# Optimization experiments

Measured on AMD Instinct MI355X. Metric: run time of the kernel, lower is better.

## Reference

```python
import jax, jax.numpy as jnp
import numpy as np
import math

B, LAT, HID, T, NCLS = 128, 128, 256, 1920, 3
EPS = 1e-5


def _ln(x, g, b):
    m = jnp.mean(x, axis=-1, keepdims=True)
    v = jnp.var(x, axis=-1, keepdims=True)
    return (x - m) * jax.lax.rsqrt(v + EPS) * g + b


def _leaky(x):
    return jax.nn.leaky_relu(x, 0.2)


def _lstm_layer(x, Wih, Whh, bih, bhh):
    # x: [T, B, D] time-major; gate order i,f,g,o (PyTorch convention)
    xw = jnp.einsum('tbd,gd->tbg', x, Wih) + bih + bhh  # precompute input projection
    Hd = Whh.shape[1]
    bsz = x.shape[1]

    def step(carry, xg):
        h, c = carry
        gates = xg + h @ Whh.T
        i, f, g, o = jnp.split(gates, 4, axis=-1)
        c = jax.nn.sigmoid(f) * c + jax.nn.sigmoid(i) * jnp.tanh(g)
        h = jax.nn.sigmoid(o) * jnp.tanh(c)
        return (h, c), h

    init = (jnp.zeros((bsz, Hd), x.dtype), jnp.zeros((bsz, Hd), x.dtype))
    _, hs = jax.lax.scan(step, init, xw)
    return hs  # [T, B, H]


def setup_inputs() -> dict:
    key = jax.random.key(0)
    ks = jax.random.split(key, 16)
    s = 0.05
    H2 = HID // 2
    d = {
        'z': jax.random.normal(ks[0], (B, LAT), jnp.float32),
        'labels': jax.random.randint(ks[1], (B,), 0, 4, jnp.int64),
        'emb_W': jax.random.normal(ks[2], (NCLS + 1, HID), jnp.float32) * s,
        'np_W': jax.random.normal(ks[3], (HID, LAT + HID), jnp.float32) * s,
        'np_b': jnp.zeros((HID,), jnp.float32),
        'np_g': jnp.ones((HID,), jnp.float32),
        'np_be': jnp.zeros((HID,), jnp.float32),
        'Wih0': jax.random.normal(ks[4], (4 * HID, 2 * HID), jnp.float32) * s,
        'Whh0': jax.random.normal(ks[5], (4 * HID, HID), jnp.float32) * s,
        'bih0': jnp.zeros((4 * HID,), jnp.float32),
        'bhh0': jnp.zeros((4 * HID,), jnp.float32),
        'Wih1': jax.random.normal(ks[6], (4 * HID, HID), jnp.float32) * s,
        'Whh1': jax.random.normal(ks[7], (4 * HID, HID), jnp.float32) * s,
        'bih1': jnp.zeros((4 * HID,), jnp.float32),
        'bhh1': jnp.zeros((4 * HID,), jnp.float32),
        'oW1': jax.random.normal(ks[8], (H2, HID), jnp.float32) * s,
        'ob1': jnp.zeros((H2,), jnp.float32),
        'og': jnp.ones((H2,), jnp.float32),
        'obe': jnp.zeros((H2,), jnp.float32),
        'oW2': jax.random.normal(ks[9], (3, H2), jnp.float32) * s,
        'ob2': jnp.zeros((3,), jnp.float32),
        'sW1': jax.random.normal(ks[10], (H2, HID), jnp.float32) * s,
        'sb1': jnp.zeros((H2,), jnp.float32),
        'sg': jnp.ones((H2,), jnp.float32),
        'sbe': jnp.zeros((H2,), jnp.float32),
        'sW2': jax.random.normal(ks[11], (1, H2), jnp.float32) * s,
        'sb2': jnp.zeros((1,), jnp.float32),
        'stress_w': jnp.array(1.8, jnp.float32),
        'amu_w': jnp.array([0.15, 0.7, 0.15], jnp.float32),
        'amu_b': jnp.array(-0.3, jnp.float32),
    }
    return d


def reference(z, labels, emb_W, np_W, np_b, np_g, np_be, Wih0, Whh0, bih0, bhh0,
              Wih1, Whh1, bih1, bhh1, oW1, ob1, og, obe, oW2, ob2,
              sW1, sb1, sg, sbe, sW2, sb2, stress_w, amu_w, amu_b):
    bsz = z.shape[0]
    emb = emb_W[labels]                                   # [B, H]
    h = _leaky(_ln(jnp.concatenate([z, emb], axis=1) @ np_W.T + np_b, np_g, np_be))
    # [B, T, 2H]
    sig_in = jnp.concatenate([
        jnp.broadcast_to(h[:, None, :], (bsz, T, HID)),
        jnp.broadcast_to(emb[:, None, :], (bsz, T, HID)),
    ], axis=2)
    x = jnp.transpose(sig_in, (1, 0, 2))                  # time-major [T, B, 2H]
    x = _lstm_layer(x, Wih0, Whh0, bih0, bhh0)
    x = _lstm_layer(x, Wih1, Whh1, bih1, bhh1)
    ch = jnp.transpose(x, (1, 0, 2))                      # [B, T, H]

    # oscillation params per sample (vectorized over batch)
    h_avg = jnp.mean(ch, axis=1)                          # [B, H]
    op = _leaky(_ln(h_avg @ oW1.T + ob1, og, obe)) @ oW2.T + ob2  # [B, 3]
    freq = 0.23 + 0.04 * jnp.tanh(op[:, 0])
    amp = 2.0 + 1.5 * jnp.tanh(op[:, 1])
    phase = math.pi * jax.nn.sigmoid(op[:, 2])
    t = jnp.linspace(0.0, 1.0, T)
    osc = amp[:, None] * jnp.sin(2.0 * math.pi * freq[:, None] * T * t[None, :] + phase[:, None])  # [B, T]

    base = jnp.tanh(_leaky(_ln(ch @ sW1.T + sb1, sg, sbe)) @ sW2.T + sb2)  # [B, T, 1]
    enhanced = 0.6 * base[..., 0] + 0.4 * osc             # [B, T]

    stressed = stress_w * enhanced                        # conv1d k=1, w=1.8
    xp = jnp.pad(enhanced, ((0, 0), (1, 1)))
    smoothed = amu_w[0] * xp[:, :-2] + amu_w[1] * xp[:, 1:-1] + amu_w[2] * xp[:, 2:] + amu_b

    lab = labels[:, None]
    out = jnp.where(lab == 1, enhanced,
          jnp.where(lab == 2, stressed,
          jnp.where(lab == 3, smoothed, jnp.zeros_like(enhanced))))
    return out[..., None]                                  # [B, T, 1]
```

## Files before the change

kernel.cpp:

```cpp
#include <hip/hip_runtime.h>

#define TSTEPS 1920
#define NB 128
#define HIDN 256
#define LATN 128
#define EPSF 1e-5f

typedef __attribute__((ext_vector_type(8))) short bf16x8;
typedef __attribute__((ext_vector_type(4))) float f32x4;

__device__ __forceinline__ unsigned short f2bf(float x) {
    unsigned u = __builtin_bit_cast(unsigned, x);
    unsigned r = (u + 0x7fffu + ((u >> 16) & 1u)) >> 16;
    return (unsigned short)r;
}
__device__ __forceinline__ float bf2f(unsigned short h) {
    unsigned u = ((unsigned)h) << 16;
    return __builtin_bit_cast(float, u);
}
__device__ __forceinline__ float fsig(float x) {
    float e = __expf(-fabsf(x));
    float s = 1.f / (1.f + e);
    return x >= 0.f ? s : 1.f - s;
}
__device__ __forceinline__ float ftanh(float x) {
    float e = __expf(-2.f * fabsf(x));
    float r = (1.f - e) / (1.f + e);
    return x >= 0.f ? r : -r;
}
__device__ __forceinline__ float fleaky(float x) { return x > 0.f ? x : 0.2f * x; }
__device__ __forceinline__ bf16x8 bcast16(uint4 v) { return __builtin_bit_cast(bf16x8, v); }

__device__ __forceinline__ unsigned aload(const unsigned* p) {
    return __hip_atomic_load(p, __ATOMIC_RELAXED, __HIP_MEMORY_SCOPE_AGENT);
}
__device__ __forceinline__ void astore(unsigned* p, unsigned v) {
    __hip_atomic_store(p, v, __ATOMIC_RELAXED, __HIP_MEMORY_SCOPE_AGENT);
}

#define MFMA(a, b, c) __builtin_amdgcn_mfma_f32_16x16x32_bf16((a), (b), (c), 0, 0, 0)

#define FLG(ph, g, s) (((ph) * 8 + (g)) * 8 + (s)) * 32
#define HPLANE(g, layer, buf) (((g) * 2 + (layer)) * 2 + (buf)) * 4096

__global__ void init_sync(unsigned* hbuf, unsigned* flags) {
    int i = blockIdx.x * 256 + threadIdx.x;
    if (i < 131072) hbuf[i] = 0u;
    if (i < 4096) flags[i] = 0u;
}

__global__ void pack_bfrag_sliced(const float* __restrict__ A, const float* __restrict__ Bsrc,
                                  int KA, int KB,
                                  unsigned short* __restrict__ hi, unsigned short* __restrict__ lo) {
    int e = blockIdx.x * 256 + threadIdx.x;
    int K = KA + KB;
    int KT = K >> 5;
    if (e >= 1024 * K) return;
    int j = e & 7;
    int l = (e >> 3) & 63;
    int r = e >> 9;
    int kt = r % KT;
    int r2 = r / KT;
    int v = r2 & 7;
    int w = r2 >> 3;
    int n = (v >> 1) * 256 + 32 * w + 16 * (v & 1) + (l & 15);
    int k = kt * 32 + (l >> 4) * 8 + j;
    float val = (k < KA) ? A[n * KA + k] : Bsrc[n * KB + (k - KA)];
    unsigned short h = f2bf(val);
    hi[e] = h;
    lo[e] = f2bf(val - bf2f(h));
}

__global__ void pack_sw1kj(const float* __restrict__ sW1, unsigned short* __restrict__ out) {
    int e = blockIdx.x * 256 + threadIdx.x;
    if (e >= 256 * 128) return;
    int j = e & 127, k = e >> 7;
    out[e] = f2bf(sW1[j * 256 + k]);
}

__global__ void pack4T(const float* __restrict__ W, int N, int K, float* __restrict__ out) {
    int e = blockIdx.x * 256 + threadIdx.x;
    if (e >= N * K) return;
    int j = e & 3;
    int rest = e >> 2;
    int n = rest % N;
    int k4 = rest / N;
    out[e] = W[n * K + 4 * k4 + j];
}

__global__ void prep_b1(const float* __restrict__ bih1, const float* __restrict__ bhh1,
                        float* __restrict__ b1sum) {
    int i = blockIdx.x * 256 + threadIdx.x;
    if (i < 1024) b1sum[i] = bih1[i] + bhh1[i];
}

__global__ void np_head(const float* __restrict__ z, const int* __restrict__ labels,
                        const float* __restrict__ emb_W, const float* __restrict__ np_W,
                        const float* __restrict__ np_b, const float* __restrict__ np_g,
                        const float* __restrict__ np_be, float* __restrict__ x_const) {
    int b = blockIdx.x;
    int j = threadIdx.x;
    __shared__ float xc[LATN + HIDN];
    __shared__ float red[8];
    int lab = labels[b];
    if (j < LATN) xc[j] = z[b * LATN + j];
    float e = emb_W[lab * HIDN + j];
    xc[LATN + j] = e;
    __syncthreads();
    float d = np_b[j];
    for (int k = 0; k < LATN + HIDN; ++k) d += xc[k] * np_W[j * (LATN + HIDN) + k];
    int lane = j & 63, wv = j >> 6;
    float s = d, s2 = d * d;
    for (int o = 1; o < 64; o <<= 1) { s += __shfl_xor(s, o); s2 += __shfl_xor(s2, o); }
    if (lane == 0) { red[wv] = s; red[4 + wv] = s2; }
    __syncthreads();
    float S = red[0] + red[1] + red[2] + red[3];
    float S2 = red[4] + red[5] + red[6] + red[7];
    float m = S * (1.f / 256.f);
    float var = S2 * (1.f / 256.f) - m * m;
    float h = fleaky((d - m) * rsqrtf(var + EPSF) * np_g[j] + np_be[j]);
    x_const[b * 512 + j] = h;
    x_const[b * 512 + 256 + j] = e;
}

__global__ void __launch_bounds__(1024) xw0_kernel(const float* __restrict__ x_const,
                                                   const float4* __restrict__ Wih0T4,
                                                   const float* __restrict__ bih0,
                                                   const float* __restrict__ bhh0,
                                                   float* __restrict__ xw0) {
    int b = blockIdx.x;
    int g = threadIdx.x;
    __shared__ float xc[512];
    if (g < 512) xc[g] = x_const[b * 512 + g];
    __syncthreads();
    const float4* xc4 = (const float4*)xc;
    float4 acc = {0.f, 0.f, 0.f, 0.f};
#pragma unroll 8
    for (int k4 = 0; k4 < 128; ++k4) {
        float4 w = Wih0T4[k4 * 1024 + g];
        float4 x = xc4[k4];
        acc.x = fmaf(w.x, x.x, acc.x);
        acc.y = fmaf(w.y, x.y, acc.y);
        acc.z = fmaf(w.z, x.z, acc.z);
        acc.w = fmaf(w.w, x.w, acc.w);
    }
    xw0[b * 1024 + g] = bih0[g] + bhh0[g] + ((acc.x + acc.y) + (acc.z + acc.w));
}

__global__ void __launch_bounds__(512, 2) lstm_coop(
    const uint4* __restrict__ whh0h, const uint4* __restrict__ whh0l,
    const uint4* __restrict__ w1h, const uint4* __restrict__ w1l,
    const unsigned short* __restrict__ sw1kj_g, const float* __restrict__ xw0g,
    const float* __restrict__ b1sum, const float* __restrict__ sb1,
    const float* __restrict__ sg, const float* __restrict__ sbe,
    const float* __restrict__ sW2, const float* __restrict__ sb2,
    unsigned* __restrict__ hbuf, unsigned* __restrict__ flags,
    float* __restrict__ base_out, float* __restrict__ hsum_out) {
    extern __shared__ char smem[];
    unsigned short* hhi = (unsigned short*)smem;
    unsigned short* hlo = (unsigned short*)(smem + 16384);
    unsigned short* sw1s = (unsigned short*)(smem + 32768);
    float* gatesL = (float*)(smem + 98304);
    float* ppart = (float*)(smem + 106752);
    char* hhiB = smem;
    char* hloB = smem + 16384;

    const int gidx = blockIdx.x & 7;
    const int W = blockIdx.x >> 3;
    const int g16 = gidx * 16;
    const int tid = threadIdx.x;
    const int l = tid & 63;
    const int v = tid >> 6;
    const int ln16 = l & 15;
    const int kg = l >> 4;

    for (int i = tid; i < 256 * 128; i += 512) sw1s[i] = sw1kj_g[i];
    for (int i = tid; i < 8192; i += 512) { hhi[i] = 0; hlo[i] = 0; }

    uint4 b0h[8], b0l[8];
#pragma unroll
    for (int kt = 0; kt < 8; ++kt) {
        int idx = ((W * 8 + v) * 8 + kt) * 64 + l;
        b0h[kt] = whh0h[idx];
        b0l[kt] = whh0l[idx];
    }
    const uint4* w1hb = w1h + ((W * 8 + v) * 16) * 64 + l;
    const uint4* w1lb = w1l + ((W * 8 + v) * 16) * 64 + l;

    const int row = tid >> 5;
    const int ul = tid & 31;
    const int ug = 32 * W + ul;
    float xwi[4], b1v[4];
#pragma unroll
    for (int gt = 0; gt < 4; ++gt) {
        xwi[gt] = xw0g[(g16 + row) * 1024 + gt * 256 + ug];
        b1v[gt] = b1sum[gt * 256 + ug];
    }
    float c0 = 0.f, c1 = 0.f, hs = 0.f;

    const float sb1a = sb1[l], sb1b = sb1[64 + l];
    const float sga = sg[l], sgb = sg[64 + l];
    const float sbea = sbe[l], sbeb = sbe[64 + l];
    const float sw2a = sW2[l], sw2b = sW2[64 + l];
    const float sb2v = sb2[0];

    unsigned* h0buf[2] = {hbuf + HPLANE(gidx, 0, 0), hbuf + HPLANE(gidx, 0, 1)};
    unsigned* h1buf[2] = {hbuf + HPLANE(gidx, 1, 0), hbuf + HPLANE(gidx, 1, 1)};
    unsigned* fl0 = flags + FLG(0, gidx, W);
    unsigned* fl1 = flags + FLG(1, gidx, W);
    unsigned* fl0base = flags + FLG(0, gidx, 0);
    unsigned* fl1base = flags + FLG(1, gidx, 0);

    const int abase = ln16 * 1024;
    const int aswz = (ln16 & 7) << 4;
    const int kgo = kg * 16;
    const int gcol = (v >> 1) * 32 + (v & 1) * 16 + ln16;
    const int hprow = 2 * W + (v & 1);
    const int hpswz = (hprow & 7) << 4;
    const int kq = v >> 1;

    __syncthreads();

    for (int t = 0; t < TSTEPS; ++t) {
        const int cur = t & 1, prev = cur ^ 1;
        {
            unsigned* src = h1buf[prev];
            for (int i = tid; i < 4096; i += 512) {
                int r_ = i >> 8, u_ = i & 255;
                unsigned val = aload(src + i);
                int off = r_ * 1024 + ((512 + 2 * u_) ^ ((r_ & 7) << 4));
                *(unsigned short*)(hhiB + off) = (unsigned short)(val >> 16);
                *(unsigned short*)(hloB + off) = (unsigned short)(val & 0xffffu);
            }
        }
        __syncthreads();
        {
            f32x4 acc = {0.f, 0.f, 0.f, 0.f};
#pragma unroll
            for (int kt = 0; kt < 8; ++kt) {
                int aoff = abase + ((kt * 64 + kgo) ^ aswz);
                bf16x8 ahi = bcast16(*(const uint4*)(hhiB + aoff));
                bf16x8 alo = bcast16(*(const uint4*)(hloB + aoff));
                bf16x8 bh = bcast16(b0h[kt]);
                bf16x8 bl = bcast16(b0l[kt]);
                acc = MFMA(ahi, bh, acc);
                acc = MFMA(alo, bh, acc);
                acc = MFMA(ahi, bl, acc);
            }
#pragma unroll
            for (int r = 0; r < 4; ++r) gatesL[(kg * 4 + r) * 132 + gcol] = acc[r];
        }
        if (t > 0) {
            float accA = 0.f, accB = 0.f;
            int hb = hprow * 1024;
#pragma unroll 4
            for (int k = kq * 64; k < kq * 64 + 64; ++k) {
                int off = hb + ((512 + 2 * k) ^ hpswz);
                float h = bf2f(*(const unsigned short*)(hhiB + off)) +
                          bf2f(*(const unsigned short*)(hloB + off));
                float wA = bf2f(sw1s[k * 128 + l]);
                float wB = bf2f(sw1s[k * 128 + 64 + l]);
                accA = fmaf(wA, h, accA);
                accB = fmaf(wB, h, accB);
            }
            ppart[(v & 1) * 512 + kq * 128 + l] = accA;
            ppart[(v & 1) * 512 + kq * 128 + 64 + l] = accB;
        }
        __syncthreads();
        {
            float i_ = gatesL[row * 132 + ul] + xwi[0];
            float f_ = gatesL[row * 132 + 32 + ul] + xwi[1];
            float g_ = gatesL[row * 132 + 64 + ul] + xwi[2];
            float o_ = gatesL[row * 132 + 96 + ul] + xwi[3];
            c0 = fsig(f_) * c0 + fsig(i_) * ftanh(g_);
            float h = fsig(o_) * ftanh(c0);
            unsigned short hh = f2bf(h);
            unsigned short ll = f2bf(h - bf2f(hh));
            astore(h0buf[cur] + row * 256 + ug, ((unsigned)hh << 16) | (unsigned)ll);
        }
        asm volatile("s_waitcnt vmcnt(0)" ::: "memory");
        __syncthreads();
        if (tid == 0) astore(fl0, (unsigned)(t + 1));
        {
            unsigned tgt = (unsigned)(t + 1);
            while (true) {
                unsigned val = (l < 8) ? aload(fl0base + l * 32) : tgt;
                if (__all((int)(val >= tgt))) break;
                __builtin_amdgcn_s_sleep(1);
            }
        }
        asm volatile("" ::: "memory");
        {
            unsigned* src = h0buf[cur];
            for (int i = tid; i < 4096; i += 512) {
                int r_ = i >> 8, u_ = i & 255;
                unsigned val = aload(src + i);
                int off = r_ * 1024 + ((2 * u_) ^ ((r_ & 7) << 4));
                *(unsigned short*)(hhiB + off) = (unsigned short)(val >> 16);
                *(unsigned short*)(hloB + off) = (unsigned short)(val & 0xffffu);
            }
        }
        __syncthreads();
        {
            f32x4 acc = {0.f, 0.f, 0.f, 0.f};
#pragma unroll 4
            for (int kt = 0; kt < 16; ++kt) {
                int aoff = abase + ((kt * 64 + kgo) ^ aswz);
                bf16x8 ahi = bcast16(*(const uint4*)(hhiB + aoff));
                bf16x8 alo = bcast16(*(const uint4*)(hloB + aoff));
                bf16x8 bh = bcast16(w1hb[kt * 64]);
                bf16x8 bl = bcast16(w1lb[kt * 64]);
                acc = MFMA(ahi, bh, acc);
                acc = MFMA(alo, bh, acc);
                acc = MFMA(ahi, bl, acc);
            }
#pragma unroll
            for (int r = 0; r < 4; ++r) gatesL[(kg * 4 + r) * 132 + gcol] = acc[r];
        }
        __syncthreads();
        {
            float i_ = gatesL[row * 132 + ul] + b1v[0];
            float f_ = gatesL[row * 132 + 32 + ul] + b1v[1];
            float g_ = gatesL[row * 132 + 64 + ul] + b1v[2];
            float o_ = gatesL[row * 132 + 96 + ul] + b1v[3];
            c1 = fsig(f_) * c1 + fsig(i_) * ftanh(g_);
            float h = fsig(o_) * ftanh(c1);
            hs += h;
            unsigned short hh = f2bf(h);
            unsigned short ll = f2bf(h - bf2f(hh));
            astore(h1buf[cur] + row * 256 + ug, ((unsigned)hh << 16) | (unsigned)ll);
        }
        if (t > 0 && v < 2) {
            float sA = sb1a, sB = sb1b;
#pragma unroll
            for (int q = 0; q < 4; ++q) {
                sA += ppart[v * 512 + q * 128 + l];
                sB += ppart[v * 512 + q * 128 + 64 + l];
            }
            float ssum = sA + sB, ssq = sA * sA + sB * sB;
#pragma unroll
            for (int o = 1; o < 64; o <<= 1) { ssum += __shfl_xor(ssum, o); ssq += __shfl_xor(ssq, o); }
            float m = ssum * (1.f / 128.f);
            float var = ssq * (1.f / 128.f) - m * m;
            float rstd = rsqrtf(var + EPSF);
            float p0 = fleaky((sA - m) * rstd * sga + sbea);
            float p1 = fleaky((sB - m) * rstd * sgb + sbeb);
            float q = p0 * sw2a + p1 * sw2b;
#pragma unroll
            for (int o = 1; o < 64; o <<= 1) q += __shfl_xor(q, o);
            if (l == 0) base_out[(g16 + 2 * W + v) * TSTEPS + (t - 1)] = ftanh(q + sb2v);
        }
        asm volatile("s_waitcnt vmcnt(0)" ::: "memory");
        __syncthreads();
        if (tid == 0) astore(fl1, (unsigned)(t + 1));
        {
            unsigned tgt = (unsigned)(t + 1);
            while (true) {
                unsigned val = (l < 8) ? aload(fl1base + l * 32) : tgt;
                if (__all((int)(val >= tgt))) break;
                __builtin_amdgcn_s_sleep(1);
            }
        }
        asm volatile("" ::: "memory");
    }
    {
        unsigned* src = h1buf[(TSTEPS - 1) & 1];
        for (int i = tid; i < 4096; i += 512) {
            int r_ = i >> 8, u_ = i & 255;
            unsigned val = aload(src + i);
            int off = r_ * 1024 + ((512 + 2 * u_) ^ ((r_ & 7) << 4));
            *(unsigned short*)(hhiB + off) = (unsigned short)(val >> 16);
            *(unsigned short*)(hloB + off) = (unsigned short)(val & 0xffffu);
        }
    }
    __syncthreads();
    {
        float accA = 0.f, accB = 0.f;
        int hb = hprow * 1024;
#pragma unroll 4
        for (int k = kq * 64; k < kq * 64 + 64; ++k) {
            int off = hb + ((512 + 2 * k) ^ hpswz);
            float h = bf2f(*(const unsigned short*)(hhiB + off)) +
                      bf2f(*(const unsigned short*)(hloB + off));
            accA = fmaf(bf2f(sw1s[k * 128 + l]), h, accA);
            accB = fmaf(bf2f(sw1s[k * 128 + 64 + l]), h, accB);
        }
        ppart[(v & 1) * 512 + kq * 128 + l] = accA;
        ppart[(v & 1) * 512 + kq * 128 + 64 + l] = accB;
    }
    __syncthreads();
    if (v < 2) {
        float sA = sb1a, sB = sb1b;
#pragma unroll
        for (int q = 0; q < 4; ++q) {
            sA += ppart[v * 512 + q * 128 + l];
            sB += ppart[v * 512 + q * 128 + 64 + l];
        }
        float ssum = sA + sB, ssq = sA * sA + sB * sB;
#pragma unroll
        for (int o = 1; o < 64; o <<= 1) { ssum += __shfl_xor(ssum, o); ssq += __shfl_xor(ssq, o); }
        float m = ssum * (1.f / 128.f);
        float var = ssq * (1.f / 128.f) - m * m;
        float rstd = rsqrtf(var + EPSF);
        float p0 = fleaky((sA - m) * rstd * sga + sbea);
        float p1 = fleaky((sB - m) * rstd * sgb + sbeb);
        float q = p0 * sw2a + p1 * sw2b;
#pragma unroll
        for (int o = 1; o < 64; o <<= 1) q += __shfl_xor(q, o);
        if (l == 0) base_out[(g16 + 2 * W + v) * TSTEPS + (TSTEPS - 1)] = ftanh(q + sb2v);
    }
    hsum_out[(g16 + row) * HIDN + ug] = hs;
}

__global__ void out_kernel(const float* __restrict__ hsum, const float* __restrict__ oW1,
                           const float* __restrict__ ob1, const float* __restrict__ og,
                           const float* __restrict__ obe, const float* __restrict__ oW2,
                           const float* __restrict__ ob2, const float* __restrict__ base,
                           const int* __restrict__ labels, const float* __restrict__ stress_w,
                           const float* __restrict__ amu_w, const float* __restrict__ amu_b,
                           float* __restrict__ out) {
    int b = blockIdx.x;
    int tid = threadIdx.x;
    int lane = tid & 63, wv = tid >> 6;
    __shared__ float havg[256];
    __shared__ float red[8];
    __shared__ float params[3];
    __shared__ float e_row[TSTEPS];
    havg[tid] = hsum[b * 256 + tid] * (1.f / (float)TSTEPS);
    __syncthreads();
    float d1 = 0.f;
    if (tid < 128) {
        d1 = ob1[tid];
        for (int k = 0; k < 256; ++k) d1 += havg[k] * oW1[tid * 256 + k];
    }
    float s = d1, s2 = d1 * d1;
    for (int o = 1; o < 64; o <<= 1) { s += __shfl_xor(s, o); s2 += __shfl_xor(s2, o); }
    if (lane == 0 && wv < 2) { red[wv] = s; red[2 + wv] = s2; }
    __syncthreads();
    float m = (red[0] + red[1]) * (1.f / 128.f);
    float var = (red[2] + red[3]) * (1.f / 128.f) - m * m;
    float rstd = rsqrtf(var + EPSF);
    float p = 0.f;
    if (tid < 128) p = fleaky((d1 - m) * rstd * og[tid] + obe[tid]);
    float q0 = tid < 128 ? p * oW2[0 * 128 + tid] : 0.f;
    float q1 = tid < 128 ? p * oW2[1 * 128 + tid] : 0.f;
    float q2 = tid < 128 ? p * oW2[2 * 128 + tid] : 0.f;
    for (int o = 1; o < 64; o <<= 1) {
        q0 += __shfl_xor(q0, o); q1 += __shfl_xor(q1, o); q2 += __shfl_xor(q2, o);
    }
    __syncthreads();
    if (lane == 0 && wv < 2) { red[wv] = q0; red[2 + wv] = q1; red[4 + wv] = q2; }
    __syncthreads();
    if (tid == 0) {
        float op0 = red[0] + red[1] + ob2[0];
        float op1 = red[2] + red[3] + ob2[1];
        float op2 = red[4] + red[5] + ob2[2];
        params[0] = 0.23f + 0.04f * ftanh(op0);
        params[1] = 2.0f + 1.5f * ftanh(op1);
        params[2] = 3.14159265358979f * fsig(op2);
    }
    __syncthreads();
    float freq = params[0], amp = params[1], ph = params[2];
    for (int t = tid; t < TSTEPS; t += 256) {
        float x = freq * ((float)TSTEPS * (float)t / (float)(TSTEPS - 1));
        x -= floorf(x);
        float osc = amp * __sinf(6.28318530717958647f * x + ph);
        e_row[t] = 0.6f * base[b * TSTEPS + t] + 0.4f * osc;
    }
    __syncthreads();
    int lab = labels[b];
    float sw = stress_w[0];
    float w0 = amu_w[0], w1 = amu_w[1], w2 = amu_w[2], ab = amu_b[0];
    for (int t = tid; t < TSTEPS; t += 256) {
        float e = e_row[t];
        float r;
        if (lab == 1) r = e;
        else if (lab == 2) r = sw * e;
        else if (lab == 3) {
            float em = t > 0 ? e_row[t - 1] : 0.f;
            float ep = t < TSTEPS - 1 ? e_row[t + 1] : 0.f;
            r = w0 * em + w1 * e + w2 * ep + ab;
        } else r = 0.f;
        out[b * TSTEPS + t] = r;
    }
}

extern "C" void kernel_launch(void* const* d_in, const int* in_sizes, int n_in,
                              void* d_out, int out_size, void* d_ws, size_t ws_size,
                              hipStream_t stream) {
    (void)in_sizes; (void)n_in; (void)out_size; (void)ws_size;
    const float* z      = (const float*)d_in[0];
    const int* labels   = (const int*)d_in[1];
    const float* emb_W  = (const float*)d_in[2];
    const float* np_W   = (const float*)d_in[3];
    const float* np_b   = (const float*)d_in[4];
    const float* np_g   = (const float*)d_in[5];
    const float* np_be  = (const float*)d_in[6];
    const float* Wih0   = (const float*)d_in[7];
    const float* Whh0   = (const float*)d_in[8];
    const float* bih0   = (const float*)d_in[9];
    const float* bhh0   = (const float*)d_in[10];
    const float* Wih1   = (const float*)d_in[11];
    const float* Whh1   = (const float*)d_in[12];
    const float* bih1   = (const float*)d_in[13];
    const float* bhh1   = (const float*)d_in[14];
    const float* oW1    = (const float*)d_in[15];
    const float* ob1    = (const float*)d_in[16];
    const float* og     = (const float*)d_in[17];
    const float* obe    = (const float*)d_in[18];
    const float* oW2    = (const float*)d_in[19];
    const float* ob2    = (const float*)d_in[20];
    const float* sW1    = (const float*)d_in[21];
    const float* sb1    = (const float*)d_in[22];
    const float* sg     = (const float*)d_in[23];
    const float* sbe    = (const float*)d_in[24];
    const float* sW2    = (const float*)d_in[25];
    const float* sb2    = (const float*)d_in[26];
    const float* stressw= (const float*)d_in[27];
    const float* amu_w  = (const float*)d_in[28];
    const float* amu_b  = (const float*)d_in[29];
    float* out = (float*)d_out;

    uint8_t* ws = (uint8_t*)d_ws;
    size_t off = 0;
    unsigned short* whh0h = (unsigned short*)(ws + off); off += (size_t)1024 * 256 * 2;
    unsigned short* whh0l = (unsigned short*)(ws + off); off += (size_t)1024 * 256 * 2;
    unsigned short* w1h   = (unsigned short*)(ws + off); off += (size_t)1024 * 512 * 2;
    unsigned short* w1l   = (unsigned short*)(ws + off); off += (size_t)1024 * 512 * 2;
    unsigned short* sw1kj = (unsigned short*)(ws + off); off += (size_t)256 * 128 * 2;
    float* Wih0T4 = (float*)(ws + off); off += (size_t)1024 * 512 * 4;
    float* x_const= (float*)(ws + off); off += (size_t)NB * 512 * 4;
    float* xw0    = (float*)(ws + off); off += (size_t)NB * 1024 * 4;
    float* b1sum  = (float*)(ws + off); off += (size_t)1024 * 4;
    float* hsum   = (float*)(ws + off); off += (size_t)NB * 256 * 4;
    float* basef  = (float*)(ws + off); off += (size_t)NB * TSTEPS * 4;
    off = (off + 255) & ~(size_t)255;
    unsigned* hbuf = (unsigned*)(ws + off); off += (size_t)131072 * 4;
    unsigned* flags= (unsigned*)(ws + off); off += (size_t)4096 * 4;

    init_sync<<<512, 256, 0, stream>>>(hbuf, flags);
    pack_bfrag_sliced<<<1024, 256, 0, stream>>>(Whh0, nullptr, 256, 0, whh0h, whh0l);
    pack_bfrag_sliced<<<2048, 256, 0, stream>>>(Wih1, Whh1, 256, 256, w1h, w1l);
    pack_sw1kj<<<128, 256, 0, stream>>>(sW1, sw1kj);
    pack4T<<<2048, 256, 0, stream>>>(Wih0, 1024, 512, Wih0T4);
    prep_b1<<<4, 256, 0, stream>>>(bih1, bhh1, b1sum);

    np_head<<<NB, 256, 0, stream>>>(z, labels, emb_W, np_W, np_b, np_g, np_be, x_const);
    xw0_kernel<<<NB, 1024, 0, stream>>>(x_const, (const float4*)Wih0T4, bih0, bhh0, xw0);
    lstm_coop<<<64, 512, 110848, stream>>>((const uint4*)whh0h, (const uint4*)whh0l,
                                           (const uint4*)w1h, (const uint4*)w1l,
                                           sw1kj, xw0, b1sum, sb1, sg, sbe, sW2, sb2,
                                           hbuf, flags, basef, hsum);
    out_kernel<<<NB, 256, 0, stream>>>(hsum, oW1, ob1, og, obe, oW2, ob2, basef, labels,
                                       stressw, amu_w, amu_b, out);
}
```

Measured before the change: 23.98 ms.

## Wavefront-pipeline LSTM layers with one grid barrier per step

Layer 1's step t-1 now runs in the same phase as layer 0's step t. Both read one staged buffer holding h0 and h1, which cuts the cross-block flag barriers from two per timestep to one. Layer-1 weights are kept in registers instead of being reloaded from global memory each step. The sW1 head projection now runs on MFMA over a repacked fragment layout instead of scalar FMA. The changes add register pressure and more LDS, and shift the head computation by one phase.

```diff
diff --git a/kernel.cpp b/kernel.cpp
--- a/kernel.cpp
+++ b/kernel.cpp
@@ -34,13 +34,16 @@
 __device__ __forceinline__ unsigned aload(const unsigned* p) {
     return __hip_atomic_load(p, __ATOMIC_RELAXED, __HIP_MEMORY_SCOPE_AGENT);
 }
+__device__ __forceinline__ unsigned long long aload64(const unsigned long long* p) {
+    return __hip_atomic_load(p, __ATOMIC_RELAXED, __HIP_MEMORY_SCOPE_AGENT);
+}
 __device__ __forceinline__ void astore(unsigned* p, unsigned v) {
     __hip_atomic_store(p, v, __ATOMIC_RELAXED, __HIP_MEMORY_SCOPE_AGENT);
 }
 
 #define MFMA(a, b, c) __builtin_amdgcn_mfma_f32_16x16x32_bf16((a), (b), (c), 0, 0, 0)
 
-#define FLG(ph, g, s) (((ph) * 8 + (g)) * 8 + (s)) * 32
+#define FLG(g, s) ((g) * 8 + (s)) * 32
 #define HPLANE(g, layer, buf) (((g) * 2 + (layer)) * 2 + (buf)) * 4096
 
 __global__ void init_sync(unsigned* hbuf, unsigned* flags) {
@@ -71,11 +74,16 @@
     lo[e] = f2bf(val - bf2f(h));
 }
 
-__global__ void pack_sw1kj(const float* __restrict__ sW1, unsigned short* __restrict__ out) {
+__global__ void pack_sw1frag(const float* __restrict__ sW1, unsigned short* __restrict__ out) {
     int e = blockIdx.x * 256 + threadIdx.x;
-    if (e >= 256 * 128) return;
-    int j = e & 127, k = e >> 7;
-    out[e] = f2bf(sW1[j * 256 + k]);
+    if (e >= 32768) return;
+    int j3 = e & 7;
+    int l = (e >> 3) & 63;
+    int r = e >> 9;
+    int kt = r & 7, w = r >> 3;
+    int n = w * 16 + (l & 15);
+    int k = kt * 32 + (l >> 4) * 8 + j3;
+    out[e] = f2bf(sW1[n * 256 + k]);
 }
 
 __global__ void pack4T(const float* __restrict__ W, int N, int K, float* __restrict__ out) {
@@ -150,20 +158,19 @@
 __global__ void __launch_bounds__(512, 2) lstm_coop(
     const uint4* __restrict__ whh0h, const uint4* __restrict__ whh0l,
     const uint4* __restrict__ w1h, const uint4* __restrict__ w1l,
-    const unsigned short* __restrict__ sw1kj_g, const float* __restrict__ xw0g,
+    const unsigned short* __restrict__ sw1f_g, const float* __restrict__ xw0g,
     const float* __restrict__ b1sum, const float* __restrict__ sb1,
     const float* __restrict__ sg, const float* __restrict__ sbe,
     const float* __restrict__ sW2, const float* __restrict__ sb2,
     unsigned* __restrict__ hbuf, unsigned* __restrict__ flags,
     float* __restrict__ base_out, float* __restrict__ hsum_out) {
     extern __shared__ char smem[];
-    unsigned short* hhi = (unsigned short*)smem;
-    unsigned short* hlo = (unsigned short*)(smem + 16384);
-    unsigned short* sw1s = (unsigned short*)(smem + 32768);
-    float* gatesL = (float*)(smem + 98304);
-    float* ppart = (float*)(smem + 106752);
-    char* hhiB = smem;
-    char* hloB = smem + 16384;
+    char* pHhi = smem;
+    char* pHlo = smem + 16384;
+    unsigned short* sw1f = (unsigned short*)(smem + 32768);
+    float* gates0 = (float*)(smem + 98304);
+    float* gates1 = (float*)(smem + 106752);
+    float* s1b = (float*)(smem + 115200);
 
     const int gidx = blockIdx.x & 7;
     const int W = blockIdx.x >> 3;
@@ -174,8 +181,8 @@
     const int ln16 = l & 15;
     const int kg = l >> 4;
 
-    for (int i = tid; i < 256 * 128; i += 512) sw1s[i] = sw1kj_g[i];
-    for (int i = tid; i < 8192; i += 512) { hhi[i] = 0; hlo[i] = 0; }
+    for (int i = tid; i < 16384; i += 512)
+        ((unsigned*)sw1f)[i] = ((const unsigned*)sw1f_g)[i];
 
     uint4 b0h[8], b0l[8];
 #pragma unroll
@@ -184,8 +191,13 @@
         b0h[kt] = whh0h[idx];
         b0l[kt] = whh0l[idx];
     }
-    const uint4* w1hb = w1h + ((W * 8 + v) * 16) * 64 + l;
-    const uint4* w1lb = w1l + ((W * 8 + v) * 16) * 64 + l;
+    uint4 w1hR[16], w1lR[16];
+#pragma unroll
+    for (int kt = 0; kt < 16; ++kt) {
+        int idx = ((W * 8 + v) * 16 + kt) * 64 + l;
+        w1hR[kt] = w1h[idx];
+        w1lR[kt] = w1l[idx];
+    }
 
     const int row = tid >> 5;
     const int ul = tid & 31;
@@ -198,218 +210,170 @@
     }
     float c0 = 0.f, c1 = 0.f, hs = 0.f;
 
-    const float sb1a = sb1[l], sb1b = sb1[64 + l];
-    const float sga = sg[l], sgb = sg[64 + l];
-    const float sbea = sbe[l], sbeb = sbe[64 + l];
-    const float sw2a = sW2[l], sw2b = sW2[64 + l];
+    const float sb1a = sb1[2 * l], sb1b = sb1[2 * l + 1];
+    const float sga = sg[2 * l], sgb = sg[2 * l + 1];
+    const float sbea = sbe[2 * l], sbeb = sbe[2 * l + 1];
+    const float sw2a = sW2[2 * l], sw2b = sW2[2 * l + 1];
     const float sb2v = sb2[0];
 
     unsigned* h0buf[2] = {hbuf + HPLANE(gidx, 0, 0), hbuf + HPLANE(gidx, 0, 1)};
     unsigned* h1buf[2] = {hbuf + HPLANE(gidx, 1, 0), hbuf + HPLANE(gidx, 1, 1)};
-    unsigned* fl0 = flags + FLG(0, gidx, W);
-    unsigned* fl1 = flags + FLG(1, gidx, W);
-    unsigned* fl0base = flags + FLG(0, gidx, 0);
-    unsigned* fl1base = flags + FLG(1, gidx, 0);
+    unsigned* fl = flags + FLG(gidx, W);
+    unsigned* flbase = flags + FLG(gidx, 0);
 
     const int abase = ln16 * 1024;
     const int aswz = (ln16 & 7) << 4;
     const int kgo = kg * 16;
     const int gcol = (v >> 1) * 32 + (v & 1) * 16 + ln16;
-    const int hprow = 2 * W + (v & 1);
-    const int hpswz = (hprow & 7) << 4;
-    const int kq = v >> 1;
-
-    __syncthreads();
-
-    for (int t = 0; t < TSTEPS; ++t) {
-        const int cur = t & 1, prev = cur ^ 1;
+
+#define WAITF(tgtv)                                                              \
+    {                                                                            \
+        unsigned tgt = (unsigned)(tgtv);                                         \
+        while (true) {                                                           \
+            unsigned val = (l < 8) ? aload(flbase + l * 32) : tgt;               \
+            if (__all((int)(val >= tgt))) break;                                 \
+            __builtin_amdgcn_s_sleep(1);                                         \
+        }                                                                        \
+    }                                                                            \
+    asm volatile("" ::: "memory");
+
+#define STAGE2(src0, src1)                                                       \
+    {                                                                            \
+        const unsigned long long* sA = (const unsigned long long*)(src0);        \
+        const unsigned long long* sB = (const unsigned long long*)(src1);        \
+        _Pragma("unroll")                                                        \
+        for (int it = 0; it < 4; ++it) {                                         \
+            int i2 = tid + 512 * it;                                             \
+            int r_ = i2 >> 7, u2 = i2 & 127;                                     \
+            int swz = (r_ & 7) << 4;                                             \
+            int off0 = r_ * 1024 + ((4 * u2) ^ swz);                             \
+            unsigned long long vA = aload64(sA + r_ * 128 + u2);                 \
+            unsigned a0 = (unsigned)vA, a1 = (unsigned)(vA >> 32);               \
+            *(unsigned*)(pHhi + off0) = (a0 >> 16) | (a1 & 0xffff0000u);         \
+            *(unsigned*)(pHlo + off0) = (a0 & 0xffffu) | (a1 << 16);             \
+            int off1 = r_ * 1024 + ((512 + 4 * u2) ^ swz);                       \
+            unsigned long long vB = aload64(sB + r_ * 128 + u2);                 \
+            unsigned e0 = (unsigned)vB, e1 = (unsigned)(vB >> 32);               \
+            *(unsigned*)(pHhi + off1) = (e0 >> 16) | (e1 & 0xffff0000u);         \
+            *(unsigned*)(pHlo + off1) = (e0 & 0xffffu) | (e1 << 16);             \
+        }                                                                        \
+    }
+
+#define HEADFIN(tout)                                                            \
+    if (v < 4) {                                                                 \
+        _Pragma("unroll")                                                        \
+        for (int r4 = 0; r4 < 4; ++r4) {                                         \
+            int hrw = v * 4 + r4;                                                \
+            float2 sv = *(const float2*)&s1b[hrw * 132 + 2 * l];                 \
+            float sA = sv.x + sb1a, sB = sv.y + sb1b;                            \
+            float ssum = sA + sB, ssq = sA * sA + sB * sB;                       \
+            _Pragma("unroll")                                                    \
+            for (int o = 1; o < 64; o <<= 1) {                                   \
+                ssum += __shfl_xor(ssum, o); ssq += __shfl_xor(ssq, o);          \
+            }                                                                    \
+            float m = ssum * (1.f / 128.f);                                      \
+            float var = ssq * (1.f / 128.f) - m * m;                             \
+            float rstd = rsqrtf(var + EPSF);                                     \
+            float p0 = fleaky((sA - m) * rstd * sga + sbea);                     \
+            float p1 = fleaky((sB - m) * rstd * sgb + sbeb);                     \
+            float qd = p0 * sw2a + p1 * sw2b;                                    \
+            _Pragma("unroll")                                                    \
+            for (int o = 1; o < 64; o <<= 1) qd += __shfl_xor(qd, o);            \
+            if (l == 0) base_out[(g16 + hrw) * TSTEPS + (tout)] = ftanh(qd + sb2v); \
+        }                                                                        \
+    }
+
+    __syncthreads();
+
+    for (int p = 0; p <= TSTEPS; ++p) {
+        WAITF(p);
+        STAGE2(h0buf[(p - 1) & 1], h1buf[p & 1]);
+        __syncthreads();
         {
-            unsigned* src = h1buf[prev];
-            for (int i = tid; i < 4096; i += 512) {
-                int r_ = i >> 8, u_ = i & 255;
-                unsigned val = aload(src + i);
-                int off = r_ * 1024 + ((512 + 2 * u_) ^ ((r_ & 7) << 4));
-                *(unsigned short*)(hhiB + off) = (unsigned short)(val >> 16);
-                *(unsigned short*)(hloB + off) = (unsigned short)(val & 0xffffu);
+            f32x4 a0 = {0.f, 0.f, 0.f, 0.f};
+            f32x4 a1 = {0.f, 0.f, 0.f, 0.f};
+            f32x4 ah = {0.f, 0.f, 0.f, 0.f};
+#pragma unroll
+            for (int kt = 0; kt < 8; ++kt) {
+                int aoff = abase + ((kt * 64 + kgo) ^ aswz);
+                bf16x8 ahi = bcast16(*(const uint4*)(pHhi + aoff));
+                bf16x8 alo = bcast16(*(const uint4*)(pHlo + aoff));
+                bf16x8 bh = bcast16(b0h[kt]);
+                bf16x8 bl = bcast16(b0l[kt]);
+                a0 = MFMA(ahi, bh, a0); a0 = MFMA(alo, bh, a0); a0 = MFMA(ahi, bl, a0);
+                bf16x8 ch = bcast16(w1hR[kt]);
+                bf16x8 cl = bcast16(w1lR[kt]);
+                a1 = MFMA(ahi, ch, a1); a1 = MFMA(alo, ch, a1); a1 = MFMA(ahi, cl, a1);
+            }
+#pragma unroll
+            for (int kt = 8; kt < 16; ++kt) {
+                int aoff = abase + ((kt * 64 + kgo) ^ aswz);
+                bf16x8 ahi = bcast16(*(const uint4*)(pHhi + aoff));
+                bf16x8 alo = bcast16(*(const uint4*)(pHlo + aoff));
+                bf16x8 ch = bcast16(w1hR[kt]);
+                bf16x8 cl = bcast16(w1lR[kt]);
+                a1 = MFMA(ahi, ch, a1); a1 = MFMA(alo, ch, a1); a1 = MFMA(ahi, cl, a1);
+                bf16x8 bsw = bcast16(*(const uint4*)&sw1f[((v * 8 + (kt - 8)) * 64 + l) * 8]);
+                ah = MFMA(ahi, bsw, ah); ah = MFMA(alo, bsw, ah);
+            }
+#pragma unroll
+            for (int r = 0; r < 4; ++r) {
+                gates0[(kg * 4 + r) * 132 + gcol] = a0[r];
+                gates1[(kg * 4 + r) * 132 + gcol] = a1[r];
+                s1b[(kg * 4 + r) * 132 + v * 16 + ln16] = ah[r];
             }
         }
         __syncthreads();
         {
-            f32x4 acc = {0.f, 0.f, 0.f, 0.f};
-#pragma unroll
-            for (int kt = 0; kt < 8; ++kt) {
-                int aoff = abase + ((kt * 64 + kgo) ^ aswz);
-                bf16x8 ahi = bcast16(*(const uint4*)(hhiB + aoff));
-                bf16x8 alo = bcast16(*(const uint4*)(hloB + aoff));
-                bf16x8 bh = bcast16(b0h[kt]);
-                bf16x8 bl = bcast16(b0l[kt]);
-                acc = MFMA(ahi, bh, acc);
-                acc = MFMA(alo, bh, acc);
-                acc = MFMA(ahi, bl, acc);
-            }
-#pragma unroll
-            for (int r = 0; r < 4; ++r) gatesL[(kg * 4 + r) * 132 + gcol] = acc[r];
-        }
-        if (t > 0) {
-            float accA = 0.f, accB = 0.f;
-            int hb = hprow * 1024;
-#pragma unroll 4
-            for (int k = kq * 64; k < kq * 64 + 64; ++k) {
-                int off = hb + ((512 + 2 * k) ^ hpswz);
-                float h = bf2f(*(const unsigned short*)(hhiB + off)) +
-                          bf2f(*(const unsigned short*)(hloB + off));
-                float wA = bf2f(sw1s[k * 128 + l]);
-                float wB = bf2f(sw1s[k * 128 + 64 + l]);
-                accA = fmaf(wA, h, accA);
-                accB = fmaf(wB, h, accB);
-            }
-            ppart[(v & 1) * 512 + kq * 128 + l] = accA;
-            ppart[(v & 1) * 512 + kq * 128 + 64 + l] = accB;
-        }
-        __syncthreads();
-        {
-            float i_ = gatesL[row * 132 + ul] + xwi[0];
-            float f_ = gatesL[row * 132 + 32 + ul] + xwi[1];
-            float g_ = gatesL[row * 132 + 64 + ul] + xwi[2];
-            float o_ = gatesL[row * 132 + 96 + ul] + xwi[3];
+            float i_ = gates0[row * 132 + ul] + xwi[0];
+            float f_ = gates0[row * 132 + 32 + ul] + xwi[1];
+            float g_ = gates0[row * 132 + 64 + ul] + xwi[2];
+            float o_ = gates0[row * 132 + 96 + ul] + xwi[3];
             c0 = fsig(f_) * c0 + fsig(i_) * ftanh(g_);
             float h = fsig(o_) * ftanh(c0);
             unsigned short hh = f2bf(h);
             unsigned short ll = f2bf(h - bf2f(hh));
-            astore(h0buf[cur] + row * 256 + ug, ((unsigned)hh << 16) | (unsigned)ll);
+            astore(h0buf[p & 1] + row * 256 + ug, ((unsigned)hh << 16) | (unsigned)ll);
         }
-        asm volatile("s_waitcnt vmcnt(0)" ::: "memory");
-        __syncthreads();
-        if (tid == 0) astore(fl0, (unsigned)(t + 1));
-        {
-            unsigned tgt = (unsigned)(t + 1);
-            while (true) {
-                unsigned val = (l < 8) ? aload(fl0base + l * 32) : tgt;
-                if (__all((int)(val >= tgt))) break;
-                __builtin_amdgcn_s_sleep(1);
-            }
-        }
-        asm volatile("" ::: "memory");
-        {
-            unsigned* src = h0buf[cur];
-            for (int i = tid; i < 4096; i += 512) {
-                int r_ = i >> 8, u_ = i & 255;
-                unsigned val = aload(src + i);
-                int off = r_ * 1024 + ((2 * u_) ^ ((r_ & 7) << 4));
-                *(unsigned short*)(hhiB + off) = (unsigned short)(val >> 16);
-                *(unsigned short*)(hloB + off) = (unsigned short)(val & 0xffffu);
-            }
-        }
-        __syncthreads();
-        {
-            f32x4 acc = {0.f, 0.f, 0.f, 0.f};
-#pragma unroll 4
-            for (int kt = 0; kt < 16; ++kt) {
-                int aoff = abase + ((kt * 64 + kgo) ^ aswz);
-                bf16x8 ahi = bcast16(*(const uint4*)(hhiB + aoff));
-                bf16x8 alo = bcast16(*(const uint4*)(hloB + aoff));
-                bf16x8 bh = bcast16(w1hb[kt * 64]);
-                bf16x8 bl = bcast16(w1lb[kt * 64]);
-                acc = MFMA(ahi, bh, acc);
-                acc = MFMA(alo, bh, acc);
-                acc = MFMA(ahi, bl, acc);
-            }
-#pragma unroll
-            for (int r = 0; r < 4; ++r) gatesL[(kg * 4 + r) * 132 + gcol] = acc[r];
-        }
-        __syncthreads();
-        {
-            float i_ = gatesL[row * 132 + ul] + b1v[0];
-            float f_ = gatesL[row * 132 + 32 + ul] + b1v[1];
-            float g_ = gatesL[row * 132 + 64 + ul] + b1v[2];
-            float o_ = gatesL[row * 132 + 96 + ul] + b1v[3];
+        if (p > 0) {
+            float i_ = gates1[row * 132 + ul] + b1v[0];
+            float f_ = gates1[row * 132 + 32 + ul] + b1v[1];
+            float g_ = gates1[row * 132 + 64 + ul] + b1v[2];
+            float o_ = gates1[row * 132 + 96 + ul] + b1v[3];
             c1 = fsig(f_) * c1 + fsig(i_) * ftanh(g_);
             float h = fsig(o_) * ftanh(c1);
             hs += h;
             unsigned short hh = f2bf(h);
             unsigned short ll = f2bf(h - bf2f(hh));
-            astore(h1buf[cur] + row * 256 + ug, ((unsigned)hh << 16) | (unsigned)ll);
-        }
-        if (t > 0 && v < 2) {
-            float sA = sb1a, sB = sb1b;
-#pragma unroll
-            for (int q = 0; q < 4; ++q) {
-                sA += ppart[v * 512 + q * 128 + l];
-                sB += ppart[v * 512 + q * 128 + 64 + l];
-            }
-            float ssum = sA + sB, ssq = sA * sA + sB * sB;
-#pragma unroll
-            for (int o = 1; o < 64; o <<= 1) { ssum += __shfl_xor(ssum, o); ssq += __shfl_xor(ssq, o); }
-            float m = ssum * (1.f / 128.f);
-            float var = ssq * (1.f / 128.f) - m * m;
-            float rstd = rsqrtf(var + EPSF);
-            float p0 = fleaky((sA - m) * rstd * sga + sbea);
-            float p1 = fleaky((sB - m) * rstd * sgb + sbeb);
-            float q = p0 * sw2a + p1 * sw2b;
-#pragma unroll
-            for (int o = 1; o < 64; o <<= 1) q += __shfl_xor(q, o);
-            if (l == 0) base_out[(g16 + 2 * W + v) * TSTEPS + (t - 1)] = ftanh(q + sb2v);
+            astore(h1buf[(p - 1) & 1] + row * 256 + ug, ((unsigned)hh << 16) | (unsigned)ll);
         }
         asm volatile("s_waitcnt vmcnt(0)" ::: "memory");
         __syncthreads();
-        if (tid == 0) astore(fl1, (unsigned)(t + 1));
-        {
-            unsigned tgt = (unsigned)(t + 1);
-            while (true) {
-                unsigned val = (l < 8) ? aload(fl1base + l * 32) : tgt;
-                if (__all((int)(val >= tgt))) break;
-                __builtin_amdgcn_s_sleep(1);
-            }
+        if (tid == 0) astore(fl, (unsigned)(p + 1));
+        if (p >= 2) HEADFIN(p - 2);
+    }
+    WAITF(TSTEPS + 1);
+    STAGE2(h0buf[(TSTEPS + 1 - 1) & 1], h1buf[(TSTEPS + 1) & 1]);
+    __syncthreads();
+    {
+        f32x4 ah = {0.f, 0.f, 0.f, 0.f};
+#pragma unroll
+        for (int kt = 8; kt < 16; ++kt) {
+            int aoff = abase + ((kt * 64 + kgo) ^ aswz);
+            bf16x8 ahi = bcast16(*(const uint4*)(pHhi + aoff));
+            bf16x8 alo = bcast16(*(const uint4*)(pHlo + aoff));
+            bf16x8 bsw = bcast16(*(const uint4*)&sw1f[((v * 8 + (kt - 8)) * 64 + l) * 8]);
+            ah = MFMA(ahi, bsw, ah); ah = MFMA(alo, bsw, ah);
         }
-        asm volatile("" ::: "memory");
-    }
-    {
-        unsigned* src = h1buf[(TSTEPS - 1) & 1];
-        for (int i = tid; i < 4096; i += 512) {
-            int r_ = i >> 8, u_ = i & 255;
-            unsigned val = aload(src + i);
-            int off = r_ * 1024 + ((512 + 2 * u_) ^ ((r_ & 7) << 4));
-            *(unsigned short*)(hhiB + off) = (unsigned short)(val >> 16);
-            *(unsigned short*)(hloB + off) = (unsigned short)(val & 0xffffu);
-        }
-    }
-    __syncthreads();
-    {
-        float accA = 0.f, accB = 0.f;
-        int hb = hprow * 1024;
-#pragma unroll 4
-        for (int k = kq * 64; k < kq * 64 + 64; ++k) {
-            int off = hb + ((512 + 2 * k) ^ hpswz);
-            float h = bf2f(*(const unsigned short*)(hhiB + off)) +
-                      bf2f(*(const unsigned short*)(hloB + off));
-            accA = fmaf(bf2f(sw1s[k * 128 + l]), h, accA);
-            accB = fmaf(bf2f(sw1s[k * 128 + 64 + l]), h, accB);
-        }
-        ppart[(v & 1) * 512 + kq * 128 + l] = accA;
-        ppart[(v & 1) * 512 + kq * 128 + 64 + l] = accB;
-    }
-    __syncthreads();
-    if (v < 2) {
-        float sA = sb1a, sB = sb1b;
-#pragma unroll
-        for (int q = 0; q < 4; ++q) {
-            sA += ppart[v * 512 + q * 128 + l];
-            sB += ppart[v * 512 + q * 128 + 64 + l];
-        }
-        float ssum = sA + sB, ssq = sA * sA + sB * sB;
-#pragma unroll
-        for (int o = 1; o < 64; o <<= 1) { ssum += __shfl_xor(ssum, o); ssq += __shfl_xor(ssq, o); }
-        float m = ssum * (1.f / 128.f);
-        float var = ssq * (1.f / 128.f) - m * m;
-        float rstd = rsqrtf(var + EPSF);
-        float p0 = fleaky((sA - m) * rstd * sga + sbea);
-        float p1 = fleaky((sB - m) * rstd * sgb + sbeb);
-        float q = p0 * sw2a + p1 * sw2b;
-#pragma unroll
-        for (int o = 1; o < 64; o <<= 1) q += __shfl_xor(q, o);
-        if (l == 0) base_out[(g16 + 2 * W + v) * TSTEPS + (TSTEPS - 1)] = ftanh(q + sb2v);
-    }
+#pragma unroll
+        for (int r = 0; r < 4; ++r) s1b[(kg * 4 + r) * 132 + v * 16 + ln16] = ah[r];
+    }
+    __syncthreads();
+    HEADFIN(TSTEPS - 1);
     hsum_out[(g16 + row) * HIDN + ug] = hs;
+#undef WAITF
+#undef STAGE2
+#undef HEADFIN
 }
 
 __global__ void out_kernel(const float* __restrict__ hsum, const float* __restrict__ oW1,
@@ -527,7 +491,7 @@
     unsigned short* whh0l = (unsigned short*)(ws + off); off += (size_t)1024 * 256 * 2;
     unsigned short* w1h   = (unsigned short*)(ws + off); off += (size_t)1024 * 512 * 2;
     unsigned short* w1l   = (unsigned short*)(ws + off); off += (size_t)1024 * 512 * 2;
-    unsigned short* sw1kj = (unsigned short*)(ws + off); off += (size_t)256 * 128 * 2;
+    unsigned short* sw1fg = (unsigned short*)(ws + off); off += (size_t)32768 * 2;
     float* Wih0T4 = (float*)(ws + off); off += (size_t)1024 * 512 * 4;
     float* x_const= (float*)(ws + off); off += (size_t)NB * 512 * 4;
     float* xw0    = (float*)(ws + off); off += (size_t)NB * 1024 * 4;
@@ -541,15 +505,15 @@
     init_sync<<<512, 256, 0, stream>>>(hbuf, flags);
     pack_bfrag_sliced<<<1024, 256, 0, stream>>>(Whh0, nullptr, 256, 0, whh0h, whh0l);
     pack_bfrag_sliced<<<2048, 256, 0, stream>>>(Wih1, Whh1, 256, 256, w1h, w1l);
-    pack_sw1kj<<<128, 256, 0, stream>>>(sW1, sw1kj);
+    pack_sw1frag<<<128, 256, 0, stream>>>(sW1, sw1fg);
     pack4T<<<2048, 256, 0, stream>>>(Wih0, 1024, 512, Wih0T4);
     prep_b1<<<4, 256, 0, stream>>>(bih1, bhh1, b1sum);
 
     np_head<<<NB, 256, 0, stream>>>(z, labels, emb_W, np_W, np_b, np_g, np_be, x_const);
     xw0_kernel<<<NB, 1024, 0, stream>>>(x_const, (const float4*)Wih0T4, bih0, bhh0, xw0);
-    lstm_coop<<<64, 512, 110848, stream>>>((const uint4*)whh0h, (const uint4*)whh0l,
+    lstm_coop<<<64, 512, 123648, stream>>>((const uint4*)whh0h, (const uint4*)whh0l,
                                            (const uint4*)w1h, (const uint4*)w1l,
-                                           sw1kj, xw0, b1sum, sb1, sg, sbe, sW2, sb2,
+                                           sw1fg, xw0, b1sum, sb1, sg, sbe, sW2, sb2,
                                            hbuf, flags, basef, hsum);
     out_kernel<<<NB, 256, 0, stream>>>(hsum, oW1, ob1, og, obe, oW2, ob2, basef, labels,
                                        stressw, amu_w, amu_b, out);
```

After: 27.60 ms. 15.1% more time.
